# Kernel optimization log

Measured on AMD Instinct MI355X. Metric: run time of the kernel, lower is better.

Reference implementation:

```python
import jax, jax.numpy as jnp
import numpy as np

BS, SEQ, DIM, DIM_MLP, E = 2, 2048, 1024, 4096, 8
STD = 0.02  # nn.init.normal_(weight, std=0.02)


def setup_inputs() -> dict:
    key = jax.random.key(0)
    k_x, k_idx, k_w1, k_w2 = jax.random.split(key, 4)
    x = jax.random.normal(k_x, (BS, SEQ, DIM), dtype=jnp.float32)
    expert_idx = jax.random.randint(k_idx, (BS, SEQ), 0, E, dtype=jnp.int32)
    W1 = jax.random.normal(k_w1, (E, DIM, DIM_MLP), dtype=jnp.float32) * STD
    b1 = jnp.zeros((E, DIM_MLP), dtype=jnp.float32)
    W2 = jax.random.normal(k_w2, (E, DIM_MLP, DIM), dtype=jnp.float32) * STD
    b2 = jnp.zeros((E, DIM), dtype=jnp.float32)
    return {"x": x, "expert_idx": expert_idx, "W1": W1, "b1": b1, "W2": W2, "b2": b2}


def reference(x, expert_idx, W1, b1, W2, b2):
    # Compute ALL experts on all tokens (faithful to the torch module).
    # h: [bs, seq, E, dim_mlp]
    h = jnp.einsum("bsd,edm->bsem", x, W1) + b1
    h = jax.nn.gelu(h, approximate=False)  # torch nn.GELU default = exact erf
    # feat: [bs, seq, E, dim]  (== torch.cat along feature dim, reshaped)
    feat = jnp.einsum("bsem,emd->bsed", h, W2) + b2
    # Per-token gather of the assigned expert's output (top-1 select).
    idx = expert_idx.astype(jnp.int32)[:, :, None, None]  # [bs, seq, 1, 1]
    out = jnp.take_along_axis(feat, idx, axis=2)[:, :, 0, :]  # [bs, seq, dim]
    return out
```

## Files before the change

kernel.cpp:

```cpp
#include <hip/hip_runtime.h>
#include <hip/hip_bf16.h>
#include <math.h>

#define TOK   4096
#define DIM   1024
#define DMLP  4096
#define NE    8
#define BM    128
#define BN    128
#define BN2   64
#define BK    128
#define PADMAX (TOK + NE * BM)
#define NTILES (PADMAX / BM)
#define MAXSUP 24

typedef __attribute__((ext_vector_type(8))) short  short8;
typedef __attribute__((ext_vector_type(4))) float  float4v;
typedef __attribute__((ext_vector_type(4))) unsigned short ushort4v;
typedef __attribute__((ext_vector_type(2))) unsigned long long ull2;

#define ASYNC16(gp, lp) __builtin_amdgcn_global_load_lds( \
    (const __attribute__((address_space(1))) unsigned int*)(gp), \
    (__attribute__((address_space(3))) unsigned int*)(lp), 16, 0, 0)

#define SWZ(R, C) (((C) & 8) | (((C) ^ (R)) & 7))
#define FRAG_OFF(R, C) ((((R) << 4) + SWZ(R, C)) << 3)
#define BOFF(C, n) ((((C) << 7) + (n)) << 3)

static __device__ __forceinline__ unsigned short f2bf(float f) {
  unsigned u = __float_as_uint(f);
  u += 0x7fffu + ((u >> 16) & 1u);
  return (unsigned short)(u >> 16);
}

static __device__ __forceinline__ float gelu_erf(float v) {
  const float x = fabsf(v) * 0.70710678118654752f;
  const float t = __builtin_amdgcn_rcpf(1.0f + 0.3275911f * x);
  const float poly = ((((1.061405429f * t - 1.453152027f) * t + 1.421413741f) * t
                       - 0.284496736f) * t + 0.254829592f) * t;
  const float erf_abs = 1.0f - poly * __expf(-x * x);
  return 0.5f * v * (1.0f + copysignf(erf_abs, v));
}

__global__ void group_kernel(const int* __restrict__ eidx,
                             int* __restrict__ perm,
                             int* __restrict__ tile_e,
                             int* __restrict__ supA,
                             int* __restrict__ supB,
                             int* __restrict__ supE) {
  __shared__ int cnt[NE], off[NE], len[NE], cur[NE];
  const int tid = threadIdx.x;
  if (tid < NE) cnt[tid] = 0;
  __syncthreads();
  for (int i = tid; i < TOK; i += 256) atomicAdd(&cnt[eidx[i]], 1);
  __syncthreads();
  if (tid == 0) {
    int o = 0;
    for (int e = 0; e < NE; e++) {
      off[e] = o;
      len[e] = ((cnt[e] + BM - 1) / BM) * BM;
      cur[e] = o;
      o += len[e];
    }
    int ns = 0;
    for (int e = 0; e < NE; e++) {
      const int nt = len[e] / BM;
      for (int p = 0; p < nt; p += 2) {
        const int pb = (p + 1 < nt) ? (p + 1) : p;
        supA[ns] = off[e] + p * BM;
        supB[ns] = off[e] + pb * BM;
        supE[ns] = e;
        ns++;
      }
    }
    for (; ns < MAXSUP; ns++) { supA[ns] = 0; supB[ns] = 0; supE[ns] = -1; }
  }
  __syncthreads();
  for (int s = tid; s < PADMAX; s += 256) perm[s] = -1;
  __syncthreads();
  for (int i = tid; i < TOK; i += 256) {
    const int e = eidx[i];
    const int p = atomicAdd(&cur[e], 1);
    perm[p] = i;
  }
  __syncthreads();
  for (int t = tid; t < NTILES; t += 256) {
    const int row = t * BM;
    int te = -1;
    for (int e = 0; e < NE; e++)
      if (row >= off[e] && row < off[e] + len[e]) te = e;
    tile_e[t] = te;
  }
}

static __device__ __forceinline__
void convpack_body(const float* __restrict__ W, unsigned short* __restrict__ WT,
                   int K, int N, int kg, int nblk, int e, int tid) {
  const int n0 = nblk * 1024 + tid * 4;
  const float* Win = W + (size_t)e * K * N + (size_t)kg * 8 * N + n0;
  unsigned short* Wout = WT + (size_t)e * K * N + ((size_t)kg * N + n0) * 8;
  float4v v[8];
#pragma unroll
  for (int j = 0; j < 8; j++) v[j] = *(const float4v*)(Win + (size_t)j * N);
#pragma unroll
  for (int q = 0; q < 4; q++) {
    short8 g;
#pragma unroll
    for (int j = 0; j < 8; j++) g[j] = (short)f2bf(v[j][q]);
    *(short8*)(Wout + q * 8) = g;
  }
}

__global__ __launch_bounds__(256)
void prep1_kernel(const float* __restrict__ W1, unsigned short* __restrict__ W1T,
                  const float* __restrict__ x, const int* __restrict__ perm,
                  unsigned short* __restrict__ xg) {
  const int bid = blockIdx.x;
  const int tid = threadIdx.x;
  if (bid < 4096) {
    convpack_body(W1, W1T, DIM, DMLP, bid & 127, (bid >> 7) & 3, bid >> 9, tid);
  } else {
    const int slot = bid - 4096;
    const int t    = perm[slot];
    ushort4v o = (ushort4v){0, 0, 0, 0};
    if (t >= 0) {
      const float4v v = *(const float4v*)(x + (size_t)t * DIM + tid * 4);
#pragma unroll
      for (int q = 0; q < 4; q++) o[q] = f2bf(v[q]);
    }
    *(ushort4v*)(xg + (size_t)slot * DIM + tid * 4) = o;
  }
}

__global__ __launch_bounds__(256)
void gemm1_kernel(const unsigned short* __restrict__ xg,
                  const unsigned short* __restrict__ W1T,
                  const float* __restrict__ b1, const int* __restrict__ tile_e,
                  unsigned short* __restrict__ h,
                  const float* __restrict__ W2, unsigned short* __restrict__ W2T) {
  const int bt = blockIdx.y;
  const int te = tile_e[bt];
  const int n0 = blockIdx.x * BN;
  const int tid = threadIdx.x;

  __shared__ __align__(16) unsigned short SMEM[2 * BM * BK];

  if (te >= 0) {
    const unsigned short* Asrc = xg + (size_t)bt * BM * DIM;
    const unsigned short* Bsrc = W1T + (size_t)te * DIM * DMLP + (size_t)n0 * 8;

    const int rr = tid >> 4, q = tid & 15;
    const int cs = SWZ(rr, q);
    const unsigned short* a0 = Asrc + (size_t)rr * DIM + cs * 8;
    const int bC = tid >> 7, bn = tid & 127;
    const unsigned short* b0 = Bsrc + ((size_t)bC * DMLP + bn) * 8;

    const int wid = tid >> 6, lane = tid & 63;
    const int wm = (wid >> 1) * 64, wn = (wid & 1) * 64;
    const int l15 = lane & 15, quad = lane >> 4;

    float4v acc[4][4];
#pragma unroll
    for (int i = 0; i < 4; i++)
#pragma unroll
      for (int j = 0; j < 4; j++) acc[i][j] = (float4v){0.f, 0.f, 0.f, 0.f};

    for (int k0 = 0; k0 < DIM; k0 += BK) {
      const int kg0 = k0 >> 3;
#pragma unroll
      for (int t = 0; t < 8; t++)
        ASYNC16(a0 + (size_t)(16 * t) * DIM + k0, &SMEM[(t * 256 + tid) * 8]);
#pragma unroll
      for (int t = 0; t < 8; t++)
        ASYNC16(b0 + (size_t)(kg0 + 2 * t) * DMLP * 8,
                &SMEM[BM * BK + (t * 256 + tid) * 8]);
      __syncthreads();

#pragma unroll
      for (int hh = 0; hh < 4; hh++) {
        short8 a[4], b[4];
        const int C = hh * 4 + quad;
#pragma unroll
        for (int i = 0; i < 4; i++)
          a[i] = *(const short8*)&SMEM[FRAG_OFF(wm + i * 16 + l15, C)];
#pragma unroll
        for (int j = 0; j < 4; j++)
          b[j] = *(const short8*)&SMEM[BM * BK + BOFF(C, wn + j * 16 + l15)];
#pragma unroll
        for (int i = 0; i < 4; i++)
#pragma unroll
          for (int j = 0; j < 4; j++)
            acc[i][j] = __builtin_amdgcn_mfma_f32_16x16x32_bf16(a[i], b[j], acc[i][j], 0, 0, 0);
      }
      __syncthreads();
    }

#pragma unroll
    for (int i = 0; i < 4; i++) {
#pragma unroll
      for (int j = 0; j < 4; j++) {
        const int colL = wn + j * 16 + l15;
        const float bias = b1[te * DMLP + n0 + colL];
#pragma unroll
        for (int r = 0; r < 4; r++) {
          const int rowL = wm + i * 16 + quad * 4 + r;
          SMEM[rowL * BN + colL] = f2bf(gelu_erf(acc[i][j][r] + bias));
        }
      }
    }
    __syncthreads();
    const int gg = tid & 15;
    const int rb = tid >> 4;
#pragma unroll
    for (int p = 0; p < 8; p++) {
      const int rowL = rb + p * 16;
      const ull2 v = *(const ull2*)&SMEM[rowL * BN + gg * 8];
      *(ull2*)&h[(size_t)(bt * BM + rowL) * DMLP + n0 + gg * 8] = v;
    }
  }

  const int fb = bt * gridDim.x + blockIdx.x;
#pragma unroll
  for (int r = 0; r < 4; r++) {
    const int c = fb + 1280 * r;
    if (c < 4096) {
      convpack_body(W2, W2T, DMLP, DIM, c & 511, 0, c >> 9, tid);
    }
  }
}

__global__ __launch_bounds__(256)
void gemm2_kernel(const unsigned short* __restrict__ h,
                  const unsigned short* __restrict__ W2T,
                  const float* __restrict__ b2, const int* __restrict__ perm,
                  const int* __restrict__ supA, const int* __restrict__ supB,
                  const int* __restrict__ supE, float* __restrict__ out) {
  const int s  = blockIdx.y;
  const int te = supE[s];
  if (te < 0) return;
  const int rowA = supA[s], rowB = supB[s];
  const int n0 = blockIdx.x * BN2;
  const int tid = threadIdx.x;

  __shared__ __align__(16) unsigned short As[256 * BK];
  __shared__ __align__(16) unsigned short Bs[16 * BN2 * 8];

  const int rr = tid >> 4, q = tid & 15;
  const int cs = SWZ(rr, q);
  const unsigned short* aA = h + (size_t)(rowA + rr) * DMLP + cs * 8;
  const unsigned short* aB = h + (size_t)(rowB + rr) * DMLP + cs * 8;
  const int bC = tid >> 6, bn = tid & 63;
  const unsigned short* b0 = W2T + (size_t)te * DMLP * DIM
                           + ((size_t)bC * DIM + n0 + bn) * 8;

  const int wid = tid >> 6, lane = tid & 63;
  const int wm = wid * 64;
  const int l15 = lane & 15, quad = lane >> 4;

  float4v acc[4][4];
#pragma unroll
  for (int i = 0; i < 4; i++)
#pragma unroll
    for (int j = 0; j < 4; j++) acc[i][j] = (float4v){0.f, 0.f, 0.f, 0.f};

  for (int k0 = 0; k0 < DMLP; k0 += BK) {
    const int kg0 = k0 >> 3;
#pragma unroll
    for (int t = 0; t < 8; t++)
      ASYNC16(aA + (size_t)(16 * t) * DMLP + k0, &As[(t * 256 + tid) * 8]);
#pragma unroll
    for (int t = 0; t < 8; t++)
      ASYNC16(aB + (size_t)(16 * t) * DMLP + k0, &As[((t + 8) * 256 + tid) * 8]);
#pragma unroll
    for (int t = 0; t < 4; t++)
      ASYNC16(b0 + (size_t)(kg0 + 4 * t) * DIM * 8, &Bs[(t * 256 + tid) * 8]);
    __syncthreads();

#pragma unroll
    for (int hh = 0; hh < 4; hh++) {
      short8 a[4], b[4];
      const int C = hh * 4 + quad;
#pragma unroll
      for (int i = 0; i < 4; i++)
        a[i] = *(const short8*)&As[FRAG_OFF(wm + i * 16 + l15, C)];
#pragma unroll
      for (int j = 0; j < 4; j++)
        b[j] = *(const short8*)&Bs[(((C) << 6) + j * 16 + l15) << 3];
#pragma unroll
      for (int i = 0; i < 4; i++)
#pragma unroll
        for (int j = 0; j < 4; j++)
          acc[i][j] = __builtin_amdgcn_mfma_f32_16x16x32_bf16(a[i], b[j], acc[i][j], 0, 0, 0);
    }
    __syncthreads();
  }

  const int halfbase = (wm < 128) ? (rowA + wm) : (rowB + (wm - 128));
#pragma unroll
  for (int i = 0; i < 4; i++) {
#pragma unroll
    for (int j = 0; j < 4; j++) {
      const int col = n0 + j * 16 + l15;
      const float bias = b2[te * DIM + col];
#pragma unroll
      for (int r = 0; r < 4; r++) {
        const int slot = halfbase + i * 16 + quad * 4 + r;
        const int t    = perm[slot];
        if (t >= 0) out[(size_t)t * DIM + col] = acc[i][j][r] + bias;
      }
    }
  }
}

extern "C" void kernel_launch(void* const* d_in, const int* in_sizes, int n_in,
                              void* d_out, int out_size, void* d_ws, size_t ws_size,
                              hipStream_t stream) {
  const float* x    = (const float*)d_in[0];
  const int*   eidx = (const int*)d_in[1];
  const float* W1   = (const float*)d_in[2];
  const float* b1   = (const float*)d_in[3];
  const float* W2   = (const float*)d_in[4];
  const float* b2   = (const float*)d_in[5];
  float* out = (float*)d_out;

  char* ws = (char*)d_ws;
  int* perm   = (int*)ws;
  int* tile_e = (int*)(ws + PADMAX * sizeof(int));
  int* supA   = (int*)(ws + 20736);
  int* supB   = (int*)(ws + 20832);
  int* supE   = (int*)(ws + 20928);
  unsigned short* xg  = (unsigned short*)(ws + 32768);
  unsigned short* h   = (unsigned short*)(ws + 32768 + 10485760);
  unsigned short* W1T = (unsigned short*)(ws + 32768 + 10485760 + 41943040);
  unsigned short* W2T = (unsigned short*)((char*)W1T + 67108864);

  group_kernel<<<1, 256, 0, stream>>>(eidx, perm, tile_e, supA, supB, supE);
  prep1_kernel<<<4096 + PADMAX, 256, 0, stream>>>(W1, W1T, x, perm, xg);
  gemm1_kernel<<<dim3(DMLP / BN, NTILES), 256, 0, stream>>>(xg, W1T, b1, tile_e, h, W2, W2T);
  gemm2_kernel<<<dim3(DIM / BN2, MAXSUP), 256, 0, stream>>>(h, W2T, b2, perm, supA, supB, supE, out);
}
```

Before: 465.3 us.

## Double-buffer LDS tiles with async prefetch in both expert GEMMs, halving BK

Both grouped GEMM kernels now keep two LDS buffers and issue the global-to-LDS async loads for the next K slice before computing on the current one. Partial vmcnt waits replace full __syncthreads drains, so memory latency can overlap with MFMA work. To fit two buffers in LDS, BK drops from 128 to 64 and the XOR swizzle is simplified to 8 column groups. In exchange there are twice as many loop iterations and barriers, and the hand-counted vmcnt values must match the number of loads per stage exactly.

```diff
diff --git a/kernel.cpp b/kernel.cpp
--- a/kernel.cpp
+++ b/kernel.cpp
@@ -9,7 +9,7 @@
 #define BM    128
 #define BN    128
 #define BN2   64
-#define BK    128
+#define BK    64
 #define PADMAX (TOK + NE * BM)
 #define NTILES (PADMAX / BM)
 #define MAXSUP 24
@@ -23,8 +23,7 @@
     (const __attribute__((address_space(1))) unsigned int*)(gp), \
     (__attribute__((address_space(3))) unsigned int*)(lp), 16, 0, 0)
 
-#define SWZ(R, C) (((C) & 8) | (((C) ^ (R)) & 7))
-#define FRAG_OFF(R, C) ((((R) << 4) + SWZ(R, C)) << 3)
+#define FRAG_OFF(R, C) ((((R) << 3) + ((C) ^ ((R) & 7))) << 3)
 #define BOFF(C, n) ((((C) << 7) + (n)) << 3)
 
 static __device__ __forceinline__ unsigned short f2bf(float f) {
@@ -143,17 +142,16 @@
   const int n0 = blockIdx.x * BN;
   const int tid = threadIdx.x;
 
-  __shared__ __align__(16) unsigned short SMEM[2 * BM * BK];
+  __shared__ __align__(16) unsigned short SMEM[32768];
 
   if (te >= 0) {
     const unsigned short* Asrc = xg + (size_t)bt * BM * DIM;
     const unsigned short* Bsrc = W1T + (size_t)te * DIM * DMLP + (size_t)n0 * 8;
 
-    const int rr = tid >> 4, q = tid & 15;
-    const int cs = SWZ(rr, q);
+    const int rr = tid >> 3;
+    const int cs = (tid & 7) ^ (rr & 7);
     const unsigned short* a0 = Asrc + (size_t)rr * DIM + cs * 8;
-    const int bC = tid >> 7, bn = tid & 127;
-    const unsigned short* b0 = Bsrc + ((size_t)bC * DMLP + bn) * 8;
+    const unsigned short* b0 = Bsrc + ((size_t)(tid >> 7) * DMLP + (tid & 127)) * 8;
 
     const int wid = tid >> 6, lane = tid & 63;
     const int wm = (wid >> 1) * 64, wn = (wid & 1) * 64;
@@ -165,35 +163,56 @@
 #pragma unroll
       for (int j = 0; j < 4; j++) acc[i][j] = (float4v){0.f, 0.f, 0.f, 0.f};
 
-    for (int k0 = 0; k0 < DIM; k0 += BK) {
-      const int kg0 = k0 >> 3;
-#pragma unroll
-      for (int t = 0; t < 8; t++)
-        ASYNC16(a0 + (size_t)(16 * t) * DIM + k0, &SMEM[(t * 256 + tid) * 8]);
-#pragma unroll
-      for (int t = 0; t < 8; t++)
-        ASYNC16(b0 + (size_t)(kg0 + 2 * t) * DMLP * 8,
-                &SMEM[BM * BK + (t * 256 + tid) * 8]);
-      __syncthreads();
-
-#pragma unroll
-      for (int hh = 0; hh < 4; hh++) {
-        short8 a[4], b[4];
-        const int C = hh * 4 + quad;
-#pragma unroll
-        for (int i = 0; i < 4; i++)
-          a[i] = *(const short8*)&SMEM[FRAG_OFF(wm + i * 16 + l15, C)];
-#pragma unroll
-        for (int j = 0; j < 4; j++)
-          b[j] = *(const short8*)&SMEM[BM * BK + BOFF(C, wn + j * 16 + l15)];
-#pragma unroll
-        for (int i = 0; i < 4; i++)
-#pragma unroll
-          for (int j = 0; j < 4; j++)
-            acc[i][j] = __builtin_amdgcn_mfma_f32_16x16x32_bf16(a[i], b[j], acc[i][j], 0, 0, 0);
+#define STAGE1(buf, k0) do {                                                   \
+    const int kg0_ = (k0) >> 3;                                                \
+    _Pragma("unroll")                                                          \
+    for (int t = 0; t < 4; t++)                                                \
+      ASYNC16(a0 + (size_t)(32 * t) * DIM + (k0),                              \
+              &SMEM[(buf) * 16384 + (t * 256 + tid) * 8]);                     \
+    _Pragma("unroll")                                                          \
+    for (int t = 0; t < 4; t++)                                                \
+      ASYNC16(b0 + (size_t)(kg0_ + 2 * t) * DMLP * 8,                          \
+              &SMEM[(buf) * 16384 + 8192 + (t * 256 + tid) * 8]);              \
+  } while (0)
+
+#define COMPUTE1(buf) do {                                                     \
+    _Pragma("unroll")                                                          \
+    for (int hh = 0; hh < 2; hh++) {                                           \
+      short8 a[4], b[4];                                                       \
+      const int C = hh * 4 + quad;                                             \
+      _Pragma("unroll")                                                        \
+      for (int i = 0; i < 4; i++)                                              \
+        a[i] = *(const short8*)&SMEM[(buf) * 16384 + FRAG_OFF(wm + i * 16 + l15, C)]; \
+      _Pragma("unroll")                                                        \
+      for (int j = 0; j < 4; j++)                                              \
+        b[j] = *(const short8*)&SMEM[(buf) * 16384 + 8192 + BOFF(C, wn + j * 16 + l15)]; \
+      _Pragma("unroll")                                                        \
+      for (int i = 0; i < 4; i++)                                              \
+        _Pragma("unroll")                                                      \
+        for (int j = 0; j < 4; j++)                                            \
+          acc[i][j] = __builtin_amdgcn_mfma_f32_16x16x32_bf16(a[i], b[j],      \
+                                                              acc[i][j], 0, 0, 0); \
+    }                                                                          \
+  } while (0)
+
+    STAGE1(0, 0);
+    int cur = 0;
+    for (int i = 0; i < DIM / BK; i++) {
+      if (i < DIM / BK - 1) {
+        STAGE1(cur ^ 1, (i + 1) * BK);
+        __builtin_amdgcn_sched_barrier(0);
+        asm volatile("s_waitcnt vmcnt(8)" ::: "memory");
+      } else {
+        asm volatile("s_waitcnt vmcnt(0)" ::: "memory");
       }
-      __syncthreads();
-    }
+      __builtin_amdgcn_s_barrier();
+      __builtin_amdgcn_sched_barrier(0);
+      COMPUTE1(cur);
+      __builtin_amdgcn_s_barrier();
+      cur ^= 1;
+    }
+#undef STAGE1
+#undef COMPUTE1
 
 #pragma unroll
     for (int i = 0; i < 4; i++) {
@@ -242,16 +261,15 @@
   const int n0 = blockIdx.x * BN2;
   const int tid = threadIdx.x;
 
-  __shared__ __align__(16) unsigned short As[256 * BK];
-  __shared__ __align__(16) unsigned short Bs[16 * BN2 * 8];
-
-  const int rr = tid >> 4, q = tid & 15;
-  const int cs = SWZ(rr, q);
+  __shared__ __align__(16) unsigned short As[2][16384];
+  __shared__ __align__(16) unsigned short Bs[2][4096];
+
+  const int rr = tid >> 3;
+  const int cs = (tid & 7) ^ (rr & 7);
   const unsigned short* aA = h + (size_t)(rowA + rr) * DMLP + cs * 8;
   const unsigned short* aB = h + (size_t)(rowB + rr) * DMLP + cs * 8;
-  const int bC = tid >> 6, bn = tid & 63;
   const unsigned short* b0 = W2T + (size_t)te * DMLP * DIM
-                           + ((size_t)bC * DIM + n0 + bn) * 8;
+                           + ((size_t)(tid >> 6) * DIM + n0 + (tid & 63)) * 8;
 
   const int wid = tid >> 6, lane = tid & 63;
   const int wm = wid * 64;
@@ -263,37 +281,60 @@
 #pragma unroll
     for (int j = 0; j < 4; j++) acc[i][j] = (float4v){0.f, 0.f, 0.f, 0.f};
 
-  for (int k0 = 0; k0 < DMLP; k0 += BK) {
-    const int kg0 = k0 >> 3;
-#pragma unroll
-    for (int t = 0; t < 8; t++)
-      ASYNC16(aA + (size_t)(16 * t) * DMLP + k0, &As[(t * 256 + tid) * 8]);
-#pragma unroll
-    for (int t = 0; t < 8; t++)
-      ASYNC16(aB + (size_t)(16 * t) * DMLP + k0, &As[((t + 8) * 256 + tid) * 8]);
-#pragma unroll
-    for (int t = 0; t < 4; t++)
-      ASYNC16(b0 + (size_t)(kg0 + 4 * t) * DIM * 8, &Bs[(t * 256 + tid) * 8]);
-    __syncthreads();
-
-#pragma unroll
-    for (int hh = 0; hh < 4; hh++) {
-      short8 a[4], b[4];
-      const int C = hh * 4 + quad;
-#pragma unroll
-      for (int i = 0; i < 4; i++)
-        a[i] = *(const short8*)&As[FRAG_OFF(wm + i * 16 + l15, C)];
-#pragma unroll
-      for (int j = 0; j < 4; j++)
-        b[j] = *(const short8*)&Bs[(((C) << 6) + j * 16 + l15) << 3];
-#pragma unroll
-      for (int i = 0; i < 4; i++)
-#pragma unroll
-        for (int j = 0; j < 4; j++)
-          acc[i][j] = __builtin_amdgcn_mfma_f32_16x16x32_bf16(a[i], b[j], acc[i][j], 0, 0, 0);
-    }
-    __syncthreads();
-  }
+#define STAGE2(buf, k0) do {                                                   \
+    const int kg0_ = (k0) >> 3;                                                \
+    _Pragma("unroll")                                                          \
+    for (int t = 0; t < 4; t++)                                                \
+      ASYNC16(aA + (size_t)(32 * t) * DMLP + (k0),                             \
+              &As[buf][(t * 256 + tid) * 8]);                                  \
+    _Pragma("unroll")                                                          \
+    for (int t = 0; t < 4; t++)                                                \
+      ASYNC16(aB + (size_t)(32 * t) * DMLP + (k0),                             \
+              &As[buf][((t + 4) * 256 + tid) * 8]);                            \
+    _Pragma("unroll")                                                          \
+    for (int t = 0; t < 2; t++)                                                \
+      ASYNC16(b0 + (size_t)(kg0_ + 4 * t) * DIM * 8,                           \
+              &Bs[buf][(t * 256 + tid) * 8]);                                  \
+  } while (0)
+
+#define COMPUTE2(buf) do {                                                     \
+    _Pragma("unroll")                                                          \
+    for (int hh = 0; hh < 2; hh++) {                                           \
+      short8 a[4], b[4];                                                       \
+      const int C = hh * 4 + quad;                                             \
+      _Pragma("unroll")                                                        \
+      for (int i = 0; i < 4; i++)                                              \
+        a[i] = *(const short8*)&As[buf][FRAG_OFF(wm + i * 16 + l15, C)];       \
+      _Pragma("unroll")                                                        \
+      for (int j = 0; j < 4; j++)                                              \
+        b[j] = *(const short8*)&Bs[buf][((C << 6) + j * 16 + l15) << 3];       \
+      _Pragma("unroll")                                                        \
+      for (int i = 0; i < 4; i++)                                              \
+        _Pragma("unroll")                                                      \
+        for (int j = 0; j < 4; j++)                                            \
+          acc[i][j] = __builtin_amdgcn_mfma_f32_16x16x32_bf16(a[i], b[j],      \
+                                                              acc[i][j], 0, 0, 0); \
+    }                                                                          \
+  } while (0)
+
+  STAGE2(0, 0);
+  int cur = 0;
+  for (int i = 0; i < DMLP / BK; i++) {
+    if (i < DMLP / BK - 1) {
+      STAGE2(cur ^ 1, (i + 1) * BK);
+      __builtin_amdgcn_sched_barrier(0);
+      asm volatile("s_waitcnt vmcnt(10)" ::: "memory");
+    } else {
+      asm volatile("s_waitcnt vmcnt(0)" ::: "memory");
+    }
+    __builtin_amdgcn_s_barrier();
+    __builtin_amdgcn_sched_barrier(0);
+    COMPUTE2(cur);
+    __builtin_amdgcn_s_barrier();
+    cur ^= 1;
+  }
+#undef STAGE2
+#undef COMPUTE2
 
   const int halfbase = (wm < 128) ? (rowA + wm) : (rowB + (wm - 128));
 #pragma unroll
```

Result: no change. 470.7 us (+1.2%).

## Rewrite gemm1 as 256x256 super-tile with double-buffered ping-pong pipeline

Applied to the files above, without the earlier changes.

gemm1 now uses 512-thread blocks computing 256x256 tiles over pairs of 128-row expert tiles (the super-tile lists already used by gemm2), with K-step 64. Global-to-LDS loads are double-buffered and issued in four phases interleaved with MFMA work, using explicit vmcnt waits, barriers and setprio to overlap loads with compute. The W2 conversion work is redistributed across the new, smaller grid. This is meant to raise data reuse and hide memory latency, at the cost of 128 KB LDS per block, higher register pressure, and fragile hand-written wait counts.

```diff
diff --git a/kernel.cpp b/kernel.cpp
--- a/kernel.cpp
+++ b/kernel.cpp
@@ -7,12 +7,11 @@
 #define DMLP  4096
 #define NE    8
 #define BM    128
-#define BN    128
 #define BN2   64
-#define BK    128
 #define PADMAX (TOK + NE * BM)
 #define NTILES (PADMAX / BM)
 #define MAXSUP 24
+#define NT1   16
 
 typedef __attribute__((ext_vector_type(8))) short  short8;
 typedef __attribute__((ext_vector_type(4))) float  float4v;
@@ -23,9 +22,9 @@
     (const __attribute__((address_space(1))) unsigned int*)(gp), \
     (__attribute__((address_space(3))) unsigned int*)(lp), 16, 0, 0)
 
-#define SWZ(R, C) (((C) & 8) | (((C) ^ (R)) & 7))
-#define FRAG_OFF(R, C) ((((R) << 4) + SWZ(R, C)) << 3)
-#define BOFF(C, n) ((((C) << 7) + (n)) << 3)
+#define FRAG_OFF64(R, C) ((((R) << 3) + ((C) ^ ((R) & 7))) << 3)
+#define SWZ128(R, C) (((C) & 8) | (((C) ^ (R)) & 7))
+#define FRAG_OFF128(R, C) ((((R) << 4) + SWZ128(R, C)) << 3)
 
 static __device__ __forceinline__ unsigned short f2bf(float f) {
   unsigned u = __float_as_uint(f);
@@ -132,100 +131,162 @@
   }
 }
 
-__global__ __launch_bounds__(256)
+__global__ __launch_bounds__(512, 2)
 void gemm1_kernel(const unsigned short* __restrict__ xg,
                   const unsigned short* __restrict__ W1T,
-                  const float* __restrict__ b1, const int* __restrict__ tile_e,
+                  const float* __restrict__ b1,
+                  const int* __restrict__ supA, const int* __restrict__ supB,
+                  const int* __restrict__ supE,
                   unsigned short* __restrict__ h,
                   const float* __restrict__ W2, unsigned short* __restrict__ W2T) {
-  const int bt = blockIdx.y;
-  const int te = tile_e[bt];
-  const int n0 = blockIdx.x * BN;
+  const int s  = blockIdx.y;
+  const int te = supE[s];
+  const int n0 = blockIdx.x * 256;
   const int tid = threadIdx.x;
 
-  __shared__ __align__(16) unsigned short SMEM[2 * BM * BK];
+  __shared__ __align__(16) unsigned short SMEM[65536];
 
   if (te >= 0) {
-    const unsigned short* Asrc = xg + (size_t)bt * BM * DIM;
-    const unsigned short* Bsrc = W1T + (size_t)te * DIM * DMLP + (size_t)n0 * 8;
-
-    const int rr = tid >> 4, q = tid & 15;
-    const int cs = SWZ(rr, q);
-    const unsigned short* a0 = Asrc + (size_t)rr * DIM + cs * 8;
-    const int bC = tid >> 7, bn = tid & 127;
-    const unsigned short* b0 = Bsrc + ((size_t)bC * DMLP + bn) * 8;
+    const int rowA = supA[s], rowB = supB[s];
+    const unsigned short* W1Te = W1T + (size_t)te * DIM * DMLP;
+
+    const int r0 = tid >> 3;
+    const int c0 = (tid & 7) ^ (r0 & 7);
+    const unsigned short* aH0 = xg + (size_t)(rowA + r0) * DIM + c0 * 8;
+    const unsigned short* aH1 = xg + (size_t)(rowB + r0) * DIM + c0 * 8;
+    const unsigned short* bP = W1Te + ((size_t)(tid >> 7) * DMLP + n0 + (tid & 127)) * 8;
 
     const int wid = tid >> 6, lane = tid & 63;
-    const int wm = (wid >> 1) * 64, wn = (wid & 1) * 64;
+    const int wr2 = wid >> 2;
+    const int wc2 = wid & 3;
     const int l15 = lane & 15, quad = lane >> 4;
 
-    float4v acc[4][4];
-#pragma unroll
-    for (int i = 0; i < 4; i++)
-#pragma unroll
-      for (int j = 0; j < 4; j++) acc[i][j] = (float4v){0.f, 0.f, 0.f, 0.f};
-
-    for (int k0 = 0; k0 < DIM; k0 += BK) {
-      const int kg0 = k0 >> 3;
-#pragma unroll
-      for (int t = 0; t < 8; t++)
-        ASYNC16(a0 + (size_t)(16 * t) * DIM + k0, &SMEM[(t * 256 + tid) * 8]);
-#pragma unroll
-      for (int t = 0; t < 8; t++)
-        ASYNC16(b0 + (size_t)(kg0 + 2 * t) * DMLP * 8,
-                &SMEM[BM * BK + (t * 256 + tid) * 8]);
-      __syncthreads();
-
-#pragma unroll
-      for (int hh = 0; hh < 4; hh++) {
-        short8 a[4], b[4];
-        const int C = hh * 4 + quad;
-#pragma unroll
-        for (int i = 0; i < 4; i++)
-          a[i] = *(const short8*)&SMEM[FRAG_OFF(wm + i * 16 + l15, C)];
-#pragma unroll
-        for (int j = 0; j < 4; j++)
-          b[j] = *(const short8*)&SMEM[BM * BK + BOFF(C, wn + j * 16 + l15)];
-#pragma unroll
-        for (int i = 0; i < 4; i++)
-#pragma unroll
-          for (int j = 0; j < 4; j++)
-            acc[i][j] = __builtin_amdgcn_mfma_f32_16x16x32_bf16(a[i], b[j], acc[i][j], 0, 0, 0);
-      }
-      __syncthreads();
-    }
-
-#pragma unroll
-    for (int i = 0; i < 4; i++) {
-#pragma unroll
-      for (int j = 0; j < 4; j++) {
-        const int colL = wn + j * 16 + l15;
-        const float bias = b1[te * DMLP + n0 + colL];
-#pragma unroll
-        for (int r = 0; r < 4; r++) {
-          const int rowL = wm + i * 16 + quad * 4 + r;
-          SMEM[rowL * BN + colL] = f2bf(gelu_erf(acc[i][j][r] + bias));
+    float4v acc[2][4][2][2];
+#pragma unroll
+    for (int a1 = 0; a1 < 2; a1++)
+#pragma unroll
+      for (int a2 = 0; a2 < 4; a2++)
+#pragma unroll
+        for (int a3 = 0; a3 < 2; a3++)
+#pragma unroll
+          for (int a4 = 0; a4 < 2; a4++)
+            acc[a1][a2][a3][a4] = (float4v){0.f, 0.f, 0.f, 0.f};
+
+#define SGA(nbuf, mh, tn) do {                                                 \
+    const unsigned short* base_ = (mh) ? aH1 : aH0;                            \
+    _Pragma("unroll")                                                          \
+    for (int t2 = 0; t2 < 2; t2++)                                             \
+      ASYNC16(base_ + (size_t)(t2 * 64) * DIM + (tn) * 64,                     \
+              &SMEM[(nbuf) * 32768 + (mh) * 8192 + (t2 * 512 + tid) * 8]);     \
+  } while (0)
+
+#define SGB(nbuf, nh, tn) do {                                                 \
+    _Pragma("unroll")                                                          \
+    for (int t2 = 0; t2 < 2; t2++)                                             \
+      ASYNC16(bP + ((size_t)((tn) * 8 + t2 * 4) * DMLP + (nh) * 128) * 8,      \
+              &SMEM[(nbuf) * 32768 + 16384 + (nh) * 8192 +                     \
+                    (t2 * 512 + tid) * 8]);                                    \
+  } while (0)
+
+#define PHASE(buf, MH, NH, STAGE_STMT, VM_STMT) do {                           \
+    short8 a_[4][2], b_[2][2];                                                 \
+    _Pragma("unroll")                                                          \
+    for (int mf = 0; mf < 4; mf++)                                             \
+      _Pragma("unroll")                                                        \
+      for (int h2 = 0; h2 < 2; h2++)                                           \
+        a_[mf][h2] = *(const short8*)&SMEM[(buf) * 32768 + (MH) * 8192 +       \
+            FRAG_OFF64(wr2 * 64 + mf * 16 + l15, h2 * 4 + quad)];              \
+    _Pragma("unroll")                                                          \
+    for (int nf = 0; nf < 2; nf++)                                             \
+      _Pragma("unroll")                                                        \
+      for (int h2 = 0; h2 < 2; h2++)                                           \
+        b_[nf][h2] = *(const short8*)&SMEM[(buf) * 32768 + 16384 +             \
+            (NH) * 8192 +                                                      \
+            ((((h2 * 4 + quad) << 7) + wc2 * 32 + nf * 16 + l15) << 3)];       \
+    STAGE_STMT;                                                                \
+    VM_STMT;                                                                   \
+    __builtin_amdgcn_s_barrier();                                              \
+    __builtin_amdgcn_sched_barrier(0);                                         \
+    __builtin_amdgcn_s_setprio(1);                                             \
+    _Pragma("unroll")                                                          \
+    for (int mf = 0; mf < 4; mf++)                                             \
+      _Pragma("unroll")                                                        \
+      for (int nf = 0; nf < 2; nf++)                                           \
+        _Pragma("unroll")                                                      \
+        for (int h2 = 0; h2 < 2; h2++)                                         \
+          acc[MH][mf][NH][nf] = __builtin_amdgcn_mfma_f32_16x16x32_bf16(       \
+              a_[mf][h2], b_[nf][h2], acc[MH][mf][NH][nf], 0, 0, 0);           \
+    __builtin_amdgcn_s_setprio(0);                                             \
+    __builtin_amdgcn_sched_barrier(0);                                         \
+    __builtin_amdgcn_s_barrier();                                              \
+  } while (0)
+
+#define VM4 asm volatile("s_waitcnt vmcnt(4)" ::: "memory")
+#define VM2 asm volatile("s_waitcnt vmcnt(2)" ::: "memory")
+#define VM0 asm volatile("s_waitcnt vmcnt(0)" ::: "memory")
+
+    SGA(0, 0, 0); SGB(0, 0, 0); SGB(0, 1, 0); SGA(0, 1, 0);
+    VM4;
+    __builtin_amdgcn_s_barrier();
+    __builtin_amdgcn_sched_barrier(0);
+
+    for (int t = 0; t < NT1 - 1; ++t) {
+      const int buf = t & 1, nbuf = buf ^ 1, tn = t + 1;
+      PHASE(buf, 0, 0, SGA(nbuf, 0, tn), VM4);
+      PHASE(buf, 0, 1, SGB(nbuf, 0, tn), VM4);
+      PHASE(buf, 1, 0, SGB(nbuf, 1, tn), (void)0);
+      PHASE(buf, 1, 1, SGA(nbuf, 1, tn), VM4);
+    }
+    {
+      const int buf = (NT1 - 1) & 1;
+      PHASE(buf, 0, 0, (void)0, VM2);
+      PHASE(buf, 0, 1, (void)0, VM0);
+      PHASE(buf, 1, 0, (void)0, (void)0);
+      PHASE(buf, 1, 1, (void)0, (void)0);
+    }
+#undef SGA
+#undef SGB
+#undef PHASE
+#undef VM4
+#undef VM2
+#undef VM0
+
+    __syncthreads();
+#pragma unroll
+    for (int nh = 0; nh < 2; nh++) {
+#pragma unroll
+      for (int nf = 0; nf < 2; nf++) {
+        const int col = nh * 128 + wc2 * 32 + nf * 16 + l15;
+        const float bias = b1[te * DMLP + n0 + col];
+#pragma unroll
+        for (int mh = 0; mh < 2; mh++) {
+#pragma unroll
+          for (int mf = 0; mf < 4; mf++) {
+#pragma unroll
+            for (int r = 0; r < 4; r++) {
+              const int row = mh * 128 + wr2 * 64 + mf * 16 + quad * 4 + r;
+              SMEM[row * 256 + col] = f2bf(gelu_erf(acc[mh][mf][nh][nf][r] + bias));
+            }
+          }
         }
       }
     }
     __syncthreads();
-    const int gg = tid & 15;
-    const int rb = tid >> 4;
-#pragma unroll
-    for (int p = 0; p < 8; p++) {
-      const int rowL = rb + p * 16;
-      const ull2 v = *(const ull2*)&SMEM[rowL * BN + gg * 8];
-      *(ull2*)&h[(size_t)(bt * BM + rowL) * DMLP + n0 + gg * 8] = v;
-    }
-  }
-
-  const int fb = bt * gridDim.x + blockIdx.x;
-#pragma unroll
-  for (int r = 0; r < 4; r++) {
-    const int c = fb + 1280 * r;
-    if (c < 4096) {
-      convpack_body(W2, W2T, DMLP, DIM, c & 511, 0, c >> 9, tid);
-    }
+#pragma unroll
+    for (int rr = 0; rr < 16; rr++) {
+      const int p = rr * 512 + tid;
+      const int row = p >> 5, g = p & 31;
+      const int grow = (row < 128) ? (rowA + row) : (rowB + row - 128);
+      const ull2 v = *(const ull2*)&SMEM[row * 256 + g * 8];
+      *(ull2*)&h[(size_t)grow * DMLP + n0 + g * 8] = v;
+    }
+  }
+
+  const int fb = blockIdx.y * gridDim.x + blockIdx.x;
+#pragma unroll
+  for (int r = 0; r < 6; ++r) {
+    const int c = fb * 2 + (tid >> 8) + 768 * r;
+    if (c < 4096) convpack_body(W2, W2T, DMLP, DIM, c & 511, 0, c >> 9, tid & 255);
   }
 }
 
@@ -242,11 +303,11 @@
   const int n0 = blockIdx.x * BN2;
   const int tid = threadIdx.x;
 
-  __shared__ __align__(16) unsigned short As[256 * BK];
+  __shared__ __align__(16) unsigned short As[256 * 128];
   __shared__ __align__(16) unsigned short Bs[16 * BN2 * 8];
 
   const int rr = tid >> 4, q = tid & 15;
-  const int cs = SWZ(rr, q);
+  const int cs = SWZ128(rr, q);
   const unsigned short* aA = h + (size_t)(rowA + rr) * DMLP + cs * 8;
   const unsigned short* aB = h + (size_t)(rowB + rr) * DMLP + cs * 8;
   const int bC = tid >> 6, bn = tid & 63;
@@ -263,7 +324,7 @@
 #pragma unroll
     for (int j = 0; j < 4; j++) acc[i][j] = (float4v){0.f, 0.f, 0.f, 0.f};
 
-  for (int k0 = 0; k0 < DMLP; k0 += BK) {
+  for (int k0 = 0; k0 < DMLP; k0 += 128) {
     const int kg0 = k0 >> 3;
 #pragma unroll
     for (int t = 0; t < 8; t++)
@@ -282,7 +343,7 @@
       const int C = hh * 4 + quad;
 #pragma unroll
       for (int i = 0; i < 4; i++)
-        a[i] = *(const short8*)&As[FRAG_OFF(wm + i * 16 + l15, C)];
+        a[i] = *(const short8*)&As[FRAG_OFF128(wm + i * 16 + l15, C)];
 #pragma unroll
       for (int j = 0; j < 4; j++)
         b[j] = *(const short8*)&Bs[(((C) << 6) + j * 16 + l15) << 3];
@@ -336,6 +397,6 @@
 
   group_kernel<<<1, 256, 0, stream>>>(eidx, perm, tile_e, supA, supB, supE);
   prep1_kernel<<<4096 + PADMAX, 256, 0, stream>>>(W1, W1T, x, perm, xg);
-  gemm1_kernel<<<dim3(DMLP / BN, NTILES), 256, 0, stream>>>(xg, W1T, b1, tile_e, h, W2, W2T);
+  gemm1_kernel<<<dim3(DMLP / 256, MAXSUP), 512, 0, stream>>>(xg, W1T, b1, supA, supB, supE, h, W2, W2T);
   gemm2_kernel<<<dim3(DIM / BN2, MAXSUP), 256, 0, stream>>>(h, W2T, b2, perm, supA, supB, supE, out);
 }
```

After: 500.7 us. +7.6%, slower.

## Replace paired 256-row supertiles in gemm2 with single 128-row tiles

Applied to the files above, without the earlier changes.

The second GEMM drops the supertile scheme, where each block covered two 128-row tiles of the same expert. Each block now handles one 128-row tile, indexed by tile_e, with four waves split 2x2 over a 128x64 output (64 rows by 32 columns per wave). This halves LDS for A and doubles the grid to NTILES rows for more parallelism and occupancy. In exchange, each W2T B tile is reused over half as many rows, so the same expert weights are streamed from memory twice as often.

```diff
diff --git a/kernel.cpp b/kernel.cpp
--- a/kernel.cpp
+++ b/kernel.cpp
@@ -12,7 +12,6 @@
 #define BK    128
 #define PADMAX (TOK + NE * BM)
 #define NTILES (PADMAX / BM)
-#define MAXSUP 24
 
 typedef __attribute__((ext_vector_type(8))) short  short8;
 typedef __attribute__((ext_vector_type(4))) float  float4v;
@@ -44,10 +43,7 @@
 
 __global__ void group_kernel(const int* __restrict__ eidx,
                              int* __restrict__ perm,
-                             int* __restrict__ tile_e,
-                             int* __restrict__ supA,
-                             int* __restrict__ supB,
-                             int* __restrict__ supE) {
+                             int* __restrict__ tile_e) {
   __shared__ int cnt[NE], off[NE], len[NE], cur[NE];
   const int tid = threadIdx.x;
   if (tid < NE) cnt[tid] = 0;
@@ -62,18 +58,6 @@
       cur[e] = o;
       o += len[e];
     }
-    int ns = 0;
-    for (int e = 0; e < NE; e++) {
-      const int nt = len[e] / BM;
-      for (int p = 0; p < nt; p += 2) {
-        const int pb = (p + 1 < nt) ? (p + 1) : p;
-        supA[ns] = off[e] + p * BM;
-        supB[ns] = off[e] + pb * BM;
-        supE[ns] = e;
-        ns++;
-      }
-    }
-    for (; ns < MAXSUP; ns++) { supA[ns] = 0; supB[ns] = 0; supE[ns] = -1; }
   }
   __syncthreads();
   for (int s = tid; s < PADMAX; s += 256) perm[s] = -1;
@@ -233,44 +217,39 @@
 void gemm2_kernel(const unsigned short* __restrict__ h,
                   const unsigned short* __restrict__ W2T,
                   const float* __restrict__ b2, const int* __restrict__ perm,
-                  const int* __restrict__ supA, const int* __restrict__ supB,
-                  const int* __restrict__ supE, float* __restrict__ out) {
-  const int s  = blockIdx.y;
-  const int te = supE[s];
+                  const int* __restrict__ tile_e, float* __restrict__ out) {
+  const int bt = blockIdx.y;
+  const int te = tile_e[bt];
   if (te < 0) return;
-  const int rowA = supA[s], rowB = supB[s];
   const int n0 = blockIdx.x * BN2;
+  const unsigned short* Asrc = h + (size_t)bt * BM * DMLP;
   const int tid = threadIdx.x;
 
-  __shared__ __align__(16) unsigned short As[256 * BK];
+  __shared__ __align__(16) unsigned short As[BM * BK];
   __shared__ __align__(16) unsigned short Bs[16 * BN2 * 8];
 
   const int rr = tid >> 4, q = tid & 15;
   const int cs = SWZ(rr, q);
-  const unsigned short* aA = h + (size_t)(rowA + rr) * DMLP + cs * 8;
-  const unsigned short* aB = h + (size_t)(rowB + rr) * DMLP + cs * 8;
+  const unsigned short* a0 = Asrc + (size_t)rr * DMLP + cs * 8;
   const int bC = tid >> 6, bn = tid & 63;
   const unsigned short* b0 = W2T + (size_t)te * DMLP * DIM
                            + ((size_t)bC * DIM + n0 + bn) * 8;
 
   const int wid = tid >> 6, lane = tid & 63;
-  const int wm = wid * 64;
+  const int wm = (wid >> 1) * 64, wn = (wid & 1) * 32;
   const int l15 = lane & 15, quad = lane >> 4;
 
-  float4v acc[4][4];
+  float4v acc[4][2];
 #pragma unroll
   for (int i = 0; i < 4; i++)
 #pragma unroll
-    for (int j = 0; j < 4; j++) acc[i][j] = (float4v){0.f, 0.f, 0.f, 0.f};
+    for (int j = 0; j < 2; j++) acc[i][j] = (float4v){0.f, 0.f, 0.f, 0.f};
 
   for (int k0 = 0; k0 < DMLP; k0 += BK) {
     const int kg0 = k0 >> 3;
 #pragma unroll
     for (int t = 0; t < 8; t++)
-      ASYNC16(aA + (size_t)(16 * t) * DMLP + k0, &As[(t * 256 + tid) * 8]);
-#pragma unroll
-    for (int t = 0; t < 8; t++)
-      ASYNC16(aB + (size_t)(16 * t) * DMLP + k0, &As[((t + 8) * 256 + tid) * 8]);
+      ASYNC16(a0 + (size_t)(16 * t) * DMLP + k0, &As[(t * 256 + tid) * 8]);
 #pragma unroll
     for (int t = 0; t < 4; t++)
       ASYNC16(b0 + (size_t)(kg0 + 4 * t) * DIM * 8, &Bs[(t * 256 + tid) * 8]);
@@ -278,33 +257,33 @@
 
 #pragma unroll
     for (int hh = 0; hh < 4; hh++) {
-      short8 a[4], b[4];
+      short8 a[4], b[2];
       const int C = hh * 4 + quad;
 #pragma unroll
       for (int i = 0; i < 4; i++)
         a[i] = *(const short8*)&As[FRAG_OFF(wm + i * 16 + l15, C)];
 #pragma unroll
-      for (int j = 0; j < 4; j++)
-        b[j] = *(const short8*)&Bs[(((C) << 6) + j * 16 + l15) << 3];
+      for (int j = 0; j < 2; j++)
+        b[j] = *(const short8*)&Bs[(((C) << 6) + wn + j * 16 + l15) << 3];
 #pragma unroll
       for (int i = 0; i < 4; i++)
 #pragma unroll
-        for (int j = 0; j < 4; j++)
+        for (int j = 0; j < 2; j++)
           acc[i][j] = __builtin_amdgcn_mfma_f32_16x16x32_bf16(a[i], b[j], acc[i][j], 0, 0, 0);
     }
     __syncthreads();
   }
 
-  const int halfbase = (wm < 128) ? (rowA + wm) : (rowB + (wm - 128));
 #pragma unroll
   for (int i = 0; i < 4; i++) {
 #pragma unroll
-    for (int j = 0; j < 4; j++) {
-      const int col = n0 + j * 16 + l15;
+    for (int j = 0; j < 2; j++) {
+      const int col = n0 + wn + j * 16 + l15;
       const float bias = b2[te * DIM + col];
 #pragma unroll
       for (int r = 0; r < 4; r++) {
-        const int slot = halfbase + i * 16 + quad * 4 + r;
+        const int row  = wm + i * 16 + quad * 4 + r;
+        const int slot = bt * BM + row;
         const int t    = perm[slot];
         if (t >= 0) out[(size_t)t * DIM + col] = acc[i][j][r] + bias;
       }
@@ -326,16 +305,13 @@
   char* ws = (char*)d_ws;
   int* perm   = (int*)ws;
   int* tile_e = (int*)(ws + PADMAX * sizeof(int));
-  int* supA   = (int*)(ws + 20736);
-  int* supB   = (int*)(ws + 20832);
-  int* supE   = (int*)(ws + 20928);
   unsigned short* xg  = (unsigned short*)(ws + 32768);
   unsigned short* h   = (unsigned short*)(ws + 32768 + 10485760);
   unsigned short* W1T = (unsigned short*)(ws + 32768 + 10485760 + 41943040);
   unsigned short* W2T = (unsigned short*)((char*)W1T + 67108864);
 
-  group_kernel<<<1, 256, 0, stream>>>(eidx, perm, tile_e, supA, supB, supE);
+  group_kernel<<<1, 256, 0, stream>>>(eidx, perm, tile_e);
   prep1_kernel<<<4096 + PADMAX, 256, 0, stream>>>(W1, W1T, x, perm, xg);
   gemm1_kernel<<<dim3(DMLP / BN, NTILES), 256, 0, stream>>>(xg, W1T, b1, tile_e, h, W2, W2T);
-  gemm2_kernel<<<dim3(DIM / BN2, MAXSUP), 256, 0, stream>>>(h, W2T, b2, perm, supA, supB, supE, out);
-}
+  gemm2_kernel<<<dim3(DIM / BN2, NTILES), 256, 0, stream>>>(h, W2T, b2, perm, tile_e, out);
+}
```

Measured after the change: 454.4 us. -2.3%, faster.
